# Optimization experiments

Measured on AMD Instinct MI355X. Metric: run time of the kernel, lower is better.

Reference implementation:

```python
import jax, jax.numpy as jnp
import numpy as np

B, T, IN_DIM, EMB = 8, 2048, 1024, 1024
NEG_INF = -1e30  # stand-in for float('-inf'); exp() underflows to 0 identically


def setup_inputs() -> dict:
    key = jax.random.key(0)
    ks = jax.random.split(key, 7)
    s = 1.0 / np.sqrt(IN_DIM)
    return {
        "x": jax.random.normal(ks[0], (B, T, IN_DIM), dtype=jnp.float32),
        "Wq": jax.random.normal(ks[1], (IN_DIM, EMB), dtype=jnp.float32) * s,
        "bq": jax.random.normal(ks[2], (EMB,), dtype=jnp.float32) * 0.01,
        "Wk": jax.random.normal(ks[3], (IN_DIM, EMB), dtype=jnp.float32) * s,
        "bk": jax.random.normal(ks[4], (EMB,), dtype=jnp.float32) * 0.01,
        "Wv": jax.random.normal(ks[5], (IN_DIM, EMB), dtype=jnp.float32) * s,
        "bv": jax.random.normal(ks[6], (EMB,), dtype=jnp.float32) * 0.01,
    }


def reference(x, Wq, bq, Wk, bk, Wv, bv):
    # projections: [B, T, EMB]
    q = x @ Wq + bq
    k = x @ Wk + bk
    v = x @ Wv + bv
    scale = jnp.asarray(EMB, x.dtype) ** 0.5
    # scores: [B, T, T]
    scores = jnp.einsum("btd,bsd->bts", q, k) / scale
    Tq = scores.shape[-2]
    causal = jnp.tril(jnp.ones((Tq, Tq), dtype=bool))  # [T, T]
    scores = jnp.where(causal, scores, jnp.asarray(NEG_INF, scores.dtype))
    # Faithful to torch.vmap(softmax): per-batch GLOBAL-matrix softmax
    # (max and sum taken over the whole [T, T] matrix, not per row).
    m = jnp.max(scores, axis=(-2, -1), keepdims=True)
    e = jnp.exp(scores - m)
    w = e / jnp.sum(e, axis=(-2, -1), keepdims=True)
    # output: [B, T, EMB]
    return jnp.einsum("bts,bsd->btd", w, v)
```

## Files before the change

### kernel.cpp

```cpp
#include <hip/hip_runtime.h>
#include <stdint.h>


#define B_   8
#define T_   2048
#define DIM  1024

typedef _Float16 f16;
typedef f16   f16x8 __attribute__((ext_vector_type(8)));
typedef f16   f16x4 __attribute__((ext_vector_type(4)));
typedef float f32x4 __attribute__((ext_vector_type(4)));

typedef const __attribute__((address_space(1))) void gvoid_t;
typedef __attribute__((address_space(3))) void lvoid_t;

__device__ __forceinline__ void stage128x32(const uint16_t* __restrict__ g, int ld,
                                            uint16_t* s, int tid) {
#pragma unroll
  for (int c = 0; c < 2; ++c) {
    int r    = (tid >> 2) + 64 * c;
    int gseg = (tid & 3) ^ ((r >> 1) & 3);
    const uint16_t* gp = g + (size_t)r * ld + gseg * 8;
    uint16_t* sp = s + c * 2048 + (tid >> 6) * 512;
    __builtin_amdgcn_global_load_lds((gvoid_t*)gp, (lvoid_t*)sp, 16, 0, 0);
  }
}

__device__ __forceinline__ f16x8 fragld(const uint16_t* s, int row, int quad) {
  int seg = quad ^ ((row >> 1) & 3);
  return *(const f16x8*)(s + row * 32 + seg * 8);
}

__device__ __forceinline__ void gemm_f16(const uint16_t* gA, const uint16_t* gB,
                                         int lda, int ldb, int ksteps,
                                         uint16_t* smem, f32x4 acc[4][4]) {
  const int tid = threadIdx.x, lane = tid & 63, wv = tid >> 6;
  const int quad = lane >> 4, l15 = lane & 15;
  const int moff = (wv >> 1) * 64, noff = (wv & 1) * 64;
  uint16_t* sA = smem;
  uint16_t* sB = smem + 4096;
#pragma unroll 1
  for (int ks = 0; ks < ksteps; ++ks) {
    if (ks) __syncthreads();
    stage128x32(gA + ks * 32, lda, sA, tid);
    stage128x32(gB + ks * 32, ldb, sB, tid);
    __syncthreads();
    f16x8 a[4], b[4];
#pragma unroll
    for (int i = 0; i < 4; ++i) {
      a[i] = fragld(sA, moff + i * 16 + l15, quad);
      b[i] = fragld(sB, noff + i * 16 + l15, quad);
    }
#pragma unroll
    for (int mi = 0; mi < 4; ++mi)
#pragma unroll
      for (int ni = 0; ni < 4; ++ni)
        acc[mi][ni] = __builtin_amdgcn_mfma_f32_16x16x32_f16(a[mi], b[ni], acc[mi][ni], 0, 0, 0);
  }
}

__device__ __forceinline__ void zero_acc(f32x4 acc[4][4]) {
  f32x4 z = {0.f, 0.f, 0.f, 0.f};
#pragma unroll
  for (int i = 0; i < 4; ++i)
#pragma unroll
    for (int j = 0; j < 4; ++j) acc[i][j] = z;
}


__device__ __forceinline__ void stage_half256(const uint16_t* __restrict__ g, int ld,
                                              uint16_t* s, int tid) {
#pragma unroll
  for (int j = 0; j < 2; ++j) {
    int r   = j * 64 + (tid >> 3);
    int seg = (tid & 7) ^ (r & 7);
    const uint16_t* gp = g + (size_t)r * ld + seg * 8;
    uint16_t* sp = s + j * 4096 + (tid >> 6) * 512;
    __builtin_amdgcn_global_load_lds((gvoid_t*)gp, (lvoid_t*)sp, 16, 0, 0);
  }
}

__device__ __forceinline__ f16x8 frag64(const uint16_t* s, int r, int gseg) {
  return *(const f16x8*)(s + r * 64 + ((gseg ^ (r & 7)) * 8));
}

__device__ __forceinline__ void lda4(const uint16_t* s, int rbase, int quad, int l15,
                                     f16x8 o[4][2]) {
#pragma unroll
  for (int mf = 0; mf < 4; ++mf) {
    int r = rbase + mf * 16 + l15;
#pragma unroll
    for (int kk = 0; kk < 2; ++kk) o[mf][kk] = frag64(s, r, kk * 4 + quad);
  }
}

__device__ __forceinline__ void ldb2(const uint16_t* s, int rbase, int quad, int l15,
                                     f16x8 o[2][2]) {
#pragma unroll
  for (int nf = 0; nf < 2; ++nf) {
    int r = rbase + nf * 16 + l15;
#pragma unroll
    for (int kk = 0; kk < 2; ++kk) o[nf][kk] = frag64(s, r, kk * 4 + quad);
  }
}

template <int M0, int N0>
__device__ __forceinline__ void mm16(f16x8 a[4][2], f16x8 b[2][2], f32x4 (&acc)[8][4]) {
#pragma unroll
  for (int kk = 0; kk < 2; ++kk)
#pragma unroll
    for (int mf = 0; mf < 4; ++mf)
#pragma unroll
      for (int nf = 0; nf < 2; ++nf)
        acc[M0 + mf][N0 + nf] = __builtin_amdgcn_mfma_f32_16x16x32_f16(
            a[mf][kk], b[nf][kk], acc[M0 + mf][N0 + nf], 0, 0, 0);
}

#define SYNC_MFMA(AA, BB, M0, N0)                      \
  __builtin_amdgcn_s_barrier();                        \
  asm volatile("s_waitcnt lgkmcnt(0)" ::: "memory");   \
  __builtin_amdgcn_s_setprio(1);                       \
  mm16<M0, N0>(AA, BB, acc);                           \
  __builtin_amdgcn_s_setprio(0);                       \
  __builtin_amdgcn_s_barrier();


__global__ void zero_lrow_kernel(float* __restrict__ lrow) {
  lrow[blockIdx.x * 256 + threadIdx.x] = 0.f;
}

__global__ void conv_x_kernel(const float* __restrict__ x, f16* __restrict__ xf) {
  size_t i = (size_t)blockIdx.x * 256 + threadIdx.x;
  float4 v = ((const float4*)x)[i];
  f16x4 o = {(f16)v.x, (f16)v.y, (f16)v.z, (f16)v.w};
  ((f16x4*)xf)[i] = o;
}

__global__ void convT_w_kernel(const float* __restrict__ Wq, const float* __restrict__ Wk,
                               const float* __restrict__ Wv, f16* __restrict__ WT) {
  __shared__ float tile[64][65];
  const int z = blockIdx.z;
  const float* W = (z == 0) ? Wq : (z == 1) ? Wk : Wv;
  const int r0 = blockIdx.x * 64, c0 = blockIdx.y * 64, tid = threadIdx.x;
#pragma unroll
  for (int i = 0; i < 16; ++i) {
    int rr = (tid >> 6) + 4 * i, cc = tid & 63;
    tile[rr][cc] = W[(size_t)(r0 + rr) * DIM + c0 + cc];
  }
  __syncthreads();
#pragma unroll
  for (int i = 0; i < 16; ++i) {
    int nn = (tid >> 6) + 4 * i, kk = tid & 63;
    WT[(size_t)z * DIM * DIM + (size_t)(c0 + nn) * DIM + r0 + kk] = (f16)tile[kk][nn];
  }
}

__global__ void reduce_z_kernel(const float* __restrict__ lrow, float* __restrict__ invZ) {
  const int b = blockIdx.x, tid = threadIdx.x;
  float s = 0.f;
  for (int i = tid; i < T_; i += 256) s += lrow[(size_t)b * T_ + i];
#pragma unroll
  for (int off = 1; off < 64; off <<= 1) s += __shfl_xor(s, off, 64);
  __shared__ float red[4];
  if ((tid & 63) == 0) red[tid >> 6] = s;
  __syncthreads();
  if (tid == 0) invZ[b] = 1.0f / (red[0] + red[1] + red[2] + red[3]);
}


__global__ __launch_bounds__(512, 2) void proj_kernel(
    const f16* __restrict__ xf, const f16* __restrict__ WT,
    const float* __restrict__ bq, const float* __restrict__ bk, const float* __restrict__ bv,
    f16* __restrict__ q, f16* __restrict__ k, f16* __restrict__ vT) {
  __shared__ uint16_t smem[65536];

  const int bid = blockIdx.x;
  const int sw  = (bid & 7) * 96 + (bid >> 3);
  const int z = sw >> 8, by = (sw >> 6) & 3, bx = sw & 63;
  const size_t arow = (size_t)bx * 256;
  const int    bcol = by * 256;
  const uint16_t* gA = (const uint16_t*)xf + arow * DIM;
  const uint16_t* gB = (const uint16_t*)WT + (size_t)z * DIM * DIM + (size_t)bcol * DIM;

  const int tid = threadIdx.x, lane = tid & 63, wv = tid >> 6;
  const int quad = lane >> 4, l15 = lane & 15;
  const int wr = wv >> 2, wc = wv & 3;

  uint16_t* sA0 = smem;
  uint16_t* sA1 = smem + 16384;
  uint16_t* sB0 = smem + 32768;
  uint16_t* sB1 = smem + 49152;

  f32x4 acc[8][4];
  {
    f32x4 zz = {0.f, 0.f, 0.f, 0.f};
#pragma unroll
    for (int i = 0; i < 8; ++i)
#pragma unroll
      for (int j = 0; j < 4; ++j) acc[i][j] = zz;
  }

  stage_half256(gA,                 DIM, sA0,        tid);
  stage_half256(gA + 128 * DIM,     DIM, sA0 + 8192, tid);
  stage_half256(gB,                 DIM, sB0,        tid);
  stage_half256(gB + 128 * DIM,     DIM, sB0 + 8192, tid);
  stage_half256(gB + 64,            DIM, sB1,        tid);
  stage_half256(gB + 64 + 128 * DIM, DIM, sB1 + 8192, tid);
  asm volatile("s_waitcnt vmcnt(4)" ::: "memory");
  __builtin_amdgcn_s_barrier();

  f16x8 alo[4][2], ahi[4][2], blo[2][2], bhi[2][2];
#pragma unroll 1
  for (int it = 0; it < 8; ++it) {
    const int t1 = 2 * it + 1;
    int t2 = 2 * it + 2; if (t2 > 15) t2 = 15;
    int t3 = 2 * it + 3; if (t3 > 15) t3 = 15;
    const uint16_t* gA1 = gA + t1 * 64;
    const uint16_t* gA2 = gA + t2 * 64;
    const uint16_t* gB2 = gB + t2 * 64;
    const uint16_t* gB3 = gB + t3 * 64;

    lda4(sA0, wr * 128,      quad, l15, alo);
    ldb2(sB0, wc * 64,       quad, l15, blo);
    stage_half256(gA1, DIM, sA1, tid);
    SYNC_MFMA(alo, blo, 0, 0)
    ldb2(sB0, wc * 64 + 32,  quad, l15, bhi);
    stage_half256(gA1 + 128 * DIM, DIM, sA1 + 8192, tid);
    SYNC_MFMA(alo, bhi, 0, 2)
    lda4(sA0, wr * 128 + 64, quad, l15, ahi);
    stage_half256(gB2, DIM, sB0, tid);
    SYNC_MFMA(ahi, bhi, 4, 2)
    stage_half256(gB2 + 128 * DIM, DIM, sB0 + 8192, tid);
    asm volatile("s_waitcnt vmcnt(4)" ::: "memory");
    SYNC_MFMA(ahi, blo, 4, 0)
    lda4(sA1, wr * 128,      quad, l15, alo);
    ldb2(sB1, wc * 64,       quad, l15, blo);
    stage_half256(gA2, DIM, sA0, tid);
    SYNC_MFMA(alo, blo, 0, 0)
    ldb2(sB1, wc * 64 + 32,  quad, l15, bhi);
    stage_half256(gA2 + 128 * DIM, DIM, sA0 + 8192, tid);
    SYNC_MFMA(alo, bhi, 0, 2)
    lda4(sA1, wr * 128 + 64, quad, l15, ahi);
    stage_half256(gB3, DIM, sB1, tid);
    SYNC_MFMA(ahi, bhi, 4, 2)
    stage_half256(gB3 + 128 * DIM, DIM, sB1 + 8192, tid);
    asm volatile("s_waitcnt vmcnt(4)" ::: "memory");
    SYNC_MFMA(ahi, blo, 4, 0)
  }

  const float* bias = (z == 0) ? bq : (z == 1) ? bk : bv;
  if (z < 2) {
    f16* O = z ? k : q;
#pragma unroll
    for (int mf = 0; mf < 8; ++mf)
#pragma unroll
      for (int nf = 0; nf < 4; ++nf) {
        int n = bcol + wc * 64 + nf * 16 + l15;
        float bb = bias[n];
        size_t row0 = arow + wr * 128 + mf * 16 + quad * 4;
#pragma unroll
        for (int r = 0; r < 4; ++r)
          O[(row0 + r) * DIM + n] = (f16)(acc[mf][nf][r] + bb);
      }
  } else {
#pragma unroll
    for (int mf = 0; mf < 8; ++mf)
#pragma unroll
      for (int nf = 0; nf < 4; ++nf) {
        int n = bcol + wc * 64 + nf * 16 + l15;
        float bb = bias[n];
        int row0 = (int)arow + wr * 128 + mf * 16 + quad * 4;
        int bb_i = row0 >> 11, t0 = row0 & 2047;
        f16x4 pk;
#pragma unroll
        for (int r = 0; r < 4; ++r) pk[r] = (f16)(acc[mf][nf][r] + bb);
        *(f16x4*)(vT + ((size_t)bb_i * DIM + n) * T_ + t0) = pk;
      }
  }
}

__global__ __launch_bounds__(256, 2) void scores_kernel(
    const f16* __restrict__ q, const f16* __restrict__ k,
    f16* __restrict__ E, float* __restrict__ lrow) {
  const int qi = blockIdx.x, ki = blockIdx.y, b = blockIdx.z;
  if (ki > qi) return;
  __shared__ uint16_t smem[8192];
  f32x4 acc[4][4];
  zero_acc(acc);
  const size_t aoff = ((size_t)b * T_ + qi * 128) * DIM;
  const size_t boff = ((size_t)b * T_ + ki * 128) * DIM;
  gemm_f16((const uint16_t*)(q + aoff), (const uint16_t*)(k + boff), DIM, DIM, DIM / 32, smem, acc);

  const int tid = threadIdx.x, lane = tid & 63, wv = tid >> 6;
  const int quad = lane >> 4, l15 = lane & 15;
  const int moff = (wv >> 1) * 64, noff = (wv & 1) * 64;
  f16*   Eb = E + (size_t)b * T_ * T_;
  float* lb = lrow + (size_t)b * T_;
  const bool diag = (ki == qi);
#pragma unroll
  for (int mi = 0; mi < 4; ++mi) {
    float rs[4] = {0.f, 0.f, 0.f, 0.f};
#pragma unroll
    for (int ni = 0; ni < 4; ++ni)
#pragma unroll
      for (int r = 0; r < 4; ++r) {
        int t = qi * 128 + moff + mi * 16 + quad * 4 + r;
        int s = ki * 128 + noff + ni * 16 + l15;
        float e = 0.f;
        if (!diag || s <= t) e = __expf(fminf(acc[mi][ni][r] * 0.03125f, 11.f));
        Eb[(size_t)t * T_ + s] = (f16)e;
        rs[r] += e;
      }
#pragma unroll
    for (int off = 1; off < 16; off <<= 1)
#pragma unroll
      for (int r = 0; r < 4; ++r) rs[r] += __shfl_xor(rs[r], off, 64);
    if (l15 == 0)
#pragma unroll
      for (int r = 0; r < 4; ++r)
        atomicAdd(&lb[qi * 128 + moff + mi * 16 + quad * 4 + r], rs[r]);
  }
}

__global__ __launch_bounds__(256, 2) void pv_kernel(
    const f16* __restrict__ E, const f16* __restrict__ vT,
    const float* __restrict__ invZ, float* __restrict__ out) {
  const int qi = blockIdx.x, nt = blockIdx.y, b = blockIdx.z;
  __shared__ uint16_t smem[8192];
  f32x4 acc[4][4];
  zero_acc(acc);
  gemm_f16((const uint16_t*)(E + ((size_t)b * T_ + qi * 128) * (size_t)T_),
           (const uint16_t*)(vT + ((size_t)b * DIM + nt * 128) * (size_t)T_),
           T_, T_, (qi + 1) * 4, smem, acc);
  const float iz = invZ[b];
  const int tid = threadIdx.x, lane = tid & 63, wv = tid >> 6;
  const int quad = lane >> 4, l15 = lane & 15;
  const int moff = (wv >> 1) * 64, noff = (wv & 1) * 64;
  float* ob = out + (size_t)b * T_ * DIM;
#pragma unroll
  for (int mi = 0; mi < 4; ++mi)
#pragma unroll
    for (int ni = 0; ni < 4; ++ni)
#pragma unroll
      for (int r = 0; r < 4; ++r) {
        int t = qi * 128 + moff + mi * 16 + quad * 4 + r;
        int n = nt * 128 + noff + ni * 16 + l15;
        ob[(size_t)t * DIM + n] = acc[mi][ni][r] * iz;
      }
}


extern "C" void kernel_launch(void* const* d_in, const int* in_sizes, int n_in,
                              void* d_out, int out_size, void* d_ws, size_t ws_size,
                              hipStream_t stream) {
  const float* x  = (const float*)d_in[0];
  const float* Wq = (const float*)d_in[1];
  const float* bq = (const float*)d_in[2];
  const float* Wk = (const float*)d_in[3];
  const float* bk = (const float*)d_in[4];
  const float* Wv = (const float*)d_in[5];
  const float* bv = (const float*)d_in[6];
  float* out = (float*)d_out;

  const size_t SZ = (size_t)B_ * T_ * DIM;
  char* ws = (char*)d_ws;
  f16*   E    = (f16*)ws;
  f16*   xf   = (f16*)ws;
  f16*   q    = (f16*)(ws + 67108864);
  f16*   k    = (f16*)(ws + 100663296);
  f16*   vT   = (f16*)(ws + 134217728);
  f16*   WT   = (f16*)(ws + 167772160);
  float* lrow = (float*)(ws + 174063616);
  float* invZ = (float*)(ws + 174129152);
  if (ws_size < (size_t)174129184) return;

  zero_lrow_kernel<<<64, 256, 0, stream>>>(lrow);
  conv_x_kernel<<<16384, 256, 0, stream>>>(x, xf);
  convT_w_kernel<<<dim3(16, 16, 3), 256, 0, stream>>>(Wq, Wk, Wv, WT);
  proj_kernel<<<dim3(768), 512, 0, stream>>>(xf, WT, bq, bk, bv, q, k, vT);
  scores_kernel<<<dim3(16, 16, 8), 256, 0, stream>>>(q, k, E, lrow);
  reduce_z_kernel<<<B_, 256, 0, stream>>>(lrow, invZ);
  pv_kernel<<<dim3(16, 8, 8), 256, 0, stream>>>(E, vT, invZ, out);
}
```

Before: 417.2 us.

## Reuse pipelined 256x256 GEMM core for scores and PV kernels

Pulls the double-buffered 8-phase 256x256 GEMM loop out of the projection kernel into a shared helper. The scores and PV kernels now use it in place of the simple 128x128 single-buffered GEMM. Scores launches only the lower-triangle tiles through a linear index with XCD-aware batch mapping, and the projection block mapping is reordered. Larger tiles and prefetching raise data reuse and MFMA utilisation, but give fewer blocks (288 and 256) and coarser causal load imbalance in PV.

```diff
diff --git a/kernel.cpp b/kernel.cpp
--- a/kernel.cpp
+++ b/kernel.cpp
@@ -13,59 +13,6 @@
 
 typedef const __attribute__((address_space(1))) void gvoid_t;
 typedef __attribute__((address_space(3))) void lvoid_t;
-
-__device__ __forceinline__ void stage128x32(const uint16_t* __restrict__ g, int ld,
-                                            uint16_t* s, int tid) {
-#pragma unroll
-  for (int c = 0; c < 2; ++c) {
-    int r    = (tid >> 2) + 64 * c;
-    int gseg = (tid & 3) ^ ((r >> 1) & 3);
-    const uint16_t* gp = g + (size_t)r * ld + gseg * 8;
-    uint16_t* sp = s + c * 2048 + (tid >> 6) * 512;
-    __builtin_amdgcn_global_load_lds((gvoid_t*)gp, (lvoid_t*)sp, 16, 0, 0);
-  }
-}
-
-__device__ __forceinline__ f16x8 fragld(const uint16_t* s, int row, int quad) {
-  int seg = quad ^ ((row >> 1) & 3);
-  return *(const f16x8*)(s + row * 32 + seg * 8);
-}
-
-__device__ __forceinline__ void gemm_f16(const uint16_t* gA, const uint16_t* gB,
-                                         int lda, int ldb, int ksteps,
-                                         uint16_t* smem, f32x4 acc[4][4]) {
-  const int tid = threadIdx.x, lane = tid & 63, wv = tid >> 6;
-  const int quad = lane >> 4, l15 = lane & 15;
-  const int moff = (wv >> 1) * 64, noff = (wv & 1) * 64;
-  uint16_t* sA = smem;
-  uint16_t* sB = smem + 4096;
-#pragma unroll 1
-  for (int ks = 0; ks < ksteps; ++ks) {
-    if (ks) __syncthreads();
-    stage128x32(gA + ks * 32, lda, sA, tid);
-    stage128x32(gB + ks * 32, ldb, sB, tid);
-    __syncthreads();
-    f16x8 a[4], b[4];
-#pragma unroll
-    for (int i = 0; i < 4; ++i) {
-      a[i] = fragld(sA, moff + i * 16 + l15, quad);
-      b[i] = fragld(sB, noff + i * 16 + l15, quad);
-    }
-#pragma unroll
-    for (int mi = 0; mi < 4; ++mi)
-#pragma unroll
-      for (int ni = 0; ni < 4; ++ni)
-        acc[mi][ni] = __builtin_amdgcn_mfma_f32_16x16x32_f16(a[mi], b[ni], acc[mi][ni], 0, 0, 0);
-  }
-}
-
-__device__ __forceinline__ void zero_acc(f32x4 acc[4][4]) {
-  f32x4 z = {0.f, 0.f, 0.f, 0.f};
-#pragma unroll
-  for (int i = 0; i < 4; ++i)
-#pragma unroll
-    for (int j = 0; j < 4; ++j) acc[i][j] = z;
-}
 
 
 __device__ __forceinline__ void stage_half256(const uint16_t* __restrict__ g, int ld,
@@ -124,6 +71,77 @@
   __builtin_amdgcn_s_setprio(0);                       \
   __builtin_amdgcn_s_barrier();
 
+__device__ __forceinline__ void gemm256_8ph(const uint16_t* __restrict__ gA,
+                                            const uint16_t* __restrict__ gB,
+                                            int lda, int ldb, int nIter,
+                                            uint16_t* smem, f32x4 (&acc)[8][4]) {
+  const int tid = threadIdx.x, lane = tid & 63, wv = tid >> 6;
+  const int quad = lane >> 4, l15 = lane & 15;
+  const int wr = wv >> 2, wc = wv & 3;
+
+  uint16_t* sA0 = smem;
+  uint16_t* sA1 = smem + 16384;
+  uint16_t* sB0 = smem + 32768;
+  uint16_t* sB1 = smem + 49152;
+
+  stage_half256(gA,                        lda, sA0,        tid);
+  stage_half256(gA + 128 * (size_t)lda,    lda, sA0 + 8192, tid);
+  stage_half256(gB,                        ldb, sB0,        tid);
+  stage_half256(gB + 128 * (size_t)ldb,    ldb, sB0 + 8192, tid);
+  stage_half256(gB + 64,                   ldb, sB1,        tid);
+  stage_half256(gB + 64 + 128 * (size_t)ldb, ldb, sB1 + 8192, tid);
+  asm volatile("s_waitcnt vmcnt(4)" ::: "memory");
+  __builtin_amdgcn_s_barrier();
+
+  f16x8 alo[4][2], ahi[4][2], blo[2][2], bhi[2][2];
+  const int tmax = 2 * nIter - 1;
+#pragma unroll 1
+  for (int it = 0; it < nIter; ++it) {
+    const int t1 = 2 * it + 1;
+    int t2 = 2 * it + 2; if (t2 > tmax) t2 = tmax;
+    int t3 = 2 * it + 3; if (t3 > tmax) t3 = tmax;
+    const uint16_t* gA1 = gA + t1 * 64;
+    const uint16_t* gA2 = gA + t2 * 64;
+    const uint16_t* gB2 = gB + t2 * 64;
+    const uint16_t* gB3 = gB + t3 * 64;
+
+    lda4(sA0, wr * 128,      quad, l15, alo);
+    ldb2(sB0, wc * 64,       quad, l15, blo);
+    stage_half256(gA1, lda, sA1, tid);
+    SYNC_MFMA(alo, blo, 0, 0)
+    ldb2(sB0, wc * 64 + 32,  quad, l15, bhi);
+    stage_half256(gA1 + 128 * (size_t)lda, lda, sA1 + 8192, tid);
+    SYNC_MFMA(alo, bhi, 0, 2)
+    lda4(sA0, wr * 128 + 64, quad, l15, ahi);
+    stage_half256(gB2, ldb, sB0, tid);
+    SYNC_MFMA(ahi, bhi, 4, 2)
+    stage_half256(gB2 + 128 * (size_t)ldb, ldb, sB0 + 8192, tid);
+    asm volatile("s_waitcnt vmcnt(4)" ::: "memory");
+    SYNC_MFMA(ahi, blo, 4, 0)
+    lda4(sA1, wr * 128,      quad, l15, alo);
+    ldb2(sB1, wc * 64,       quad, l15, blo);
+    stage_half256(gA2, lda, sA0, tid);
+    SYNC_MFMA(alo, blo, 0, 0)
+    ldb2(sB1, wc * 64 + 32,  quad, l15, bhi);
+    stage_half256(gA2 + 128 * (size_t)lda, lda, sA0 + 8192, tid);
+    SYNC_MFMA(alo, bhi, 0, 2)
+    lda4(sA1, wr * 128 + 64, quad, l15, ahi);
+    stage_half256(gB3, ldb, sB1, tid);
+    SYNC_MFMA(ahi, bhi, 4, 2)
+    stage_half256(gB3 + 128 * (size_t)ldb, ldb, sB1 + 8192, tid);
+    asm volatile("s_waitcnt vmcnt(4)" ::: "memory");
+    SYNC_MFMA(ahi, blo, 4, 0)
+  }
+}
+
+__device__ __forceinline__ void zero_acc8(f32x4 (&acc)[8][4]) {
+  f32x4 z = {0.f, 0.f, 0.f, 0.f};
+#pragma unroll
+  for (int i = 0; i < 8; ++i)
+#pragma unroll
+    for (int j = 0; j < 4; ++j) acc[i][j] = z;
+}
+
 
 __global__ void zero_lrow_kernel(float* __restrict__ lrow) {
   lrow[blockIdx.x * 256 + threadIdx.x] = 0.f;
@@ -175,80 +193,23 @@
   __shared__ uint16_t smem[65536];
 
   const int bid = blockIdx.x;
-  const int sw  = (bid & 7) * 96 + (bid >> 3);
-  const int z = sw >> 8, by = (sw >> 6) & 3, bx = sw & 63;
+  const int xcd = bid & 7, local = bid >> 3;
+  const int bx = xcd * 8 + (local & 7);
+  const int zy = local >> 3;
+  const int z = zy >> 2, by = zy & 3;
   const size_t arow = (size_t)bx * 256;
   const int    bcol = by * 256;
-  const uint16_t* gA = (const uint16_t*)xf + arow * DIM;
-  const uint16_t* gB = (const uint16_t*)WT + (size_t)z * DIM * DIM + (size_t)bcol * DIM;
-
+
+  f32x4 acc[8][4];
+  zero_acc8(acc);
+  gemm256_8ph((const uint16_t*)xf + arow * DIM,
+              (const uint16_t*)WT + (size_t)z * DIM * DIM + (size_t)bcol * DIM,
+              DIM, DIM, 8, smem, acc);
+
+  const float* bias = (z == 0) ? bq : (z == 1) ? bk : bv;
   const int tid = threadIdx.x, lane = tid & 63, wv = tid >> 6;
   const int quad = lane >> 4, l15 = lane & 15;
   const int wr = wv >> 2, wc = wv & 3;
-
-  uint16_t* sA0 = smem;
-  uint16_t* sA1 = smem + 16384;
-  uint16_t* sB0 = smem + 32768;
-  uint16_t* sB1 = smem + 49152;
-
-  f32x4 acc[8][4];
-  {
-    f32x4 zz = {0.f, 0.f, 0.f, 0.f};
-#pragma unroll
-    for (int i = 0; i < 8; ++i)
-#pragma unroll
-      for (int j = 0; j < 4; ++j) acc[i][j] = zz;
-  }
-
-  stage_half256(gA,                 DIM, sA0,        tid);
-  stage_half256(gA + 128 * DIM,     DIM, sA0 + 8192, tid);
-  stage_half256(gB,                 DIM, sB0,        tid);
-  stage_half256(gB + 128 * DIM,     DIM, sB0 + 8192, tid);
-  stage_half256(gB + 64,            DIM, sB1,        tid);
-  stage_half256(gB + 64 + 128 * DIM, DIM, sB1 + 8192, tid);
-  asm volatile("s_waitcnt vmcnt(4)" ::: "memory");
-  __builtin_amdgcn_s_barrier();
-
-  f16x8 alo[4][2], ahi[4][2], blo[2][2], bhi[2][2];
-#pragma unroll 1
-  for (int it = 0; it < 8; ++it) {
-    const int t1 = 2 * it + 1;
-    int t2 = 2 * it + 2; if (t2 > 15) t2 = 15;
-    int t3 = 2 * it + 3; if (t3 > 15) t3 = 15;
-    const uint16_t* gA1 = gA + t1 * 64;
-    const uint16_t* gA2 = gA + t2 * 64;
-    const uint16_t* gB2 = gB + t2 * 64;
-    const uint16_t* gB3 = gB + t3 * 64;
-
-    lda4(sA0, wr * 128,      quad, l15, alo);
-    ldb2(sB0, wc * 64,       quad, l15, blo);
-    stage_half256(gA1, DIM, sA1, tid);
-    SYNC_MFMA(alo, blo, 0, 0)
-    ldb2(sB0, wc * 64 + 32,  quad, l15, bhi);
-    stage_half256(gA1 + 128 * DIM, DIM, sA1 + 8192, tid);
-    SYNC_MFMA(alo, bhi, 0, 2)
-    lda4(sA0, wr * 128 + 64, quad, l15, ahi);
-    stage_half256(gB2, DIM, sB0, tid);
-    SYNC_MFMA(ahi, bhi, 4, 2)
-    stage_half256(gB2 + 128 * DIM, DIM, sB0 + 8192, tid);
-    asm volatile("s_waitcnt vmcnt(4)" ::: "memory");
-    SYNC_MFMA(ahi, blo, 4, 0)
-    lda4(sA1, wr * 128,      quad, l15, alo);
-    ldb2(sB1, wc * 64,       quad, l15, blo);
-    stage_half256(gA2, DIM, sA0, tid);
-    SYNC_MFMA(alo, blo, 0, 0)
-    ldb2(sB1, wc * 64 + 32,  quad, l15, bhi);
-    stage_half256(gA2 + 128 * DIM, DIM, sA0 + 8192, tid);
-    SYNC_MFMA(alo, bhi, 0, 2)
-    lda4(sA1, wr * 128 + 64, quad, l15, ahi);
-    stage_half256(gB3, DIM, sB1, tid);
-    SYNC_MFMA(ahi, bhi, 4, 2)
-    stage_half256(gB3 + 128 * DIM, DIM, sB1 + 8192, tid);
-    asm volatile("s_waitcnt vmcnt(4)" ::: "memory");
-    SYNC_MFMA(ahi, blo, 4, 0)
-  }
-
-  const float* bias = (z == 0) ? bq : (z == 1) ? bk : bv;
   if (z < 2) {
     f16* O = z ? k : q;
 #pragma unroll
@@ -279,35 +240,39 @@
   }
 }
 
-__global__ __launch_bounds__(256, 2) void scores_kernel(
+__global__ __launch_bounds__(512, 2) void scores_kernel(
     const f16* __restrict__ q, const f16* __restrict__ k,
     f16* __restrict__ E, float* __restrict__ lrow) {
-  const int qi = blockIdx.x, ki = blockIdx.y, b = blockIdx.z;
-  if (ki > qi) return;
-  __shared__ uint16_t smem[8192];
-  f32x4 acc[4][4];
-  zero_acc(acc);
-  const size_t aoff = ((size_t)b * T_ + qi * 128) * DIM;
-  const size_t boff = ((size_t)b * T_ + ki * 128) * DIM;
-  gemm_f16((const uint16_t*)(q + aoff), (const uint16_t*)(k + boff), DIM, DIM, DIM / 32, smem, acc);
+  __shared__ uint16_t smem[65536];
+  const int bid = blockIdx.x;
+  const int b = bid & 7, tri = bid >> 3;
+  int qi = 0;
+  while ((qi + 1) * (qi + 2) / 2 <= tri) ++qi;
+  const int ki = tri - qi * (qi + 1) / 2;
+
+  f32x4 acc[8][4];
+  zero_acc8(acc);
+  gemm256_8ph((const uint16_t*)(q + ((size_t)b * T_ + qi * 256) * DIM),
+              (const uint16_t*)(k + ((size_t)b * T_ + ki * 256) * DIM),
+              DIM, DIM, 8, smem, acc);
 
   const int tid = threadIdx.x, lane = tid & 63, wv = tid >> 6;
   const int quad = lane >> 4, l15 = lane & 15;
-  const int moff = (wv >> 1) * 64, noff = (wv & 1) * 64;
+  const int wr = wv >> 2, wc = wv & 3;
   f16*   Eb = E + (size_t)b * T_ * T_;
   float* lb = lrow + (size_t)b * T_;
   const bool diag = (ki == qi);
 #pragma unroll
-  for (int mi = 0; mi < 4; ++mi) {
+  for (int mf = 0; mf < 8; ++mf) {
     float rs[4] = {0.f, 0.f, 0.f, 0.f};
 #pragma unroll
-    for (int ni = 0; ni < 4; ++ni)
+    for (int nf = 0; nf < 4; ++nf)
 #pragma unroll
       for (int r = 0; r < 4; ++r) {
-        int t = qi * 128 + moff + mi * 16 + quad * 4 + r;
-        int s = ki * 128 + noff + ni * 16 + l15;
+        int t = qi * 256 + wr * 128 + mf * 16 + quad * 4 + r;
+        int s = ki * 256 + wc * 64 + nf * 16 + l15;
         float e = 0.f;
-        if (!diag || s <= t) e = __expf(fminf(acc[mi][ni][r] * 0.03125f, 11.f));
+        if (!diag || s <= t) e = __expf(fminf(acc[mf][nf][r] * 0.03125f, 11.f));
         Eb[(size_t)t * T_ + s] = (f16)e;
         rs[r] += e;
       }
@@ -318,34 +283,38 @@
     if (l15 == 0)
 #pragma unroll
       for (int r = 0; r < 4; ++r)
-        atomicAdd(&lb[qi * 128 + moff + mi * 16 + quad * 4 + r], rs[r]);
-  }
-}
-
-__global__ __launch_bounds__(256, 2) void pv_kernel(
+        atomicAdd(&lb[qi * 256 + wr * 128 + mf * 16 + quad * 4 + r], rs[r]);
+  }
+}
+
+__global__ __launch_bounds__(512, 2) void pv_kernel(
     const f16* __restrict__ E, const f16* __restrict__ vT,
     const float* __restrict__ invZ, float* __restrict__ out) {
-  const int qi = blockIdx.x, nt = blockIdx.y, b = blockIdx.z;
-  __shared__ uint16_t smem[8192];
-  f32x4 acc[4][4];
-  zero_acc(acc);
-  gemm_f16((const uint16_t*)(E + ((size_t)b * T_ + qi * 128) * (size_t)T_),
-           (const uint16_t*)(vT + ((size_t)b * DIM + nt * 128) * (size_t)T_),
-           T_, T_, (qi + 1) * 4, smem, acc);
+  __shared__ uint16_t smem[65536];
+  const int bid = blockIdx.x;
+  const int b = bid & 7, local = bid >> 3;
+  const int qi = local & 7, nt = local >> 3;
+
+  f32x4 acc[8][4];
+  zero_acc8(acc);
+  gemm256_8ph((const uint16_t*)(E + ((size_t)b * T_ + qi * 256) * (size_t)T_),
+              (const uint16_t*)(vT + ((size_t)b * DIM + nt * 256) * (size_t)T_),
+              T_, T_, (qi + 1) * 2, smem, acc);
+
   const float iz = invZ[b];
   const int tid = threadIdx.x, lane = tid & 63, wv = tid >> 6;
   const int quad = lane >> 4, l15 = lane & 15;
-  const int moff = (wv >> 1) * 64, noff = (wv & 1) * 64;
+  const int wr = wv >> 2, wc = wv & 3;
   float* ob = out + (size_t)b * T_ * DIM;
 #pragma unroll
-  for (int mi = 0; mi < 4; ++mi)
-#pragma unroll
-    for (int ni = 0; ni < 4; ++ni)
+  for (int mf = 0; mf < 8; ++mf)
+#pragma unroll
+    for (int nf = 0; nf < 4; ++nf)
 #pragma unroll
       for (int r = 0; r < 4; ++r) {
-        int t = qi * 128 + moff + mi * 16 + quad * 4 + r;
-        int n = nt * 128 + noff + ni * 16 + l15;
-        ob[(size_t)t * DIM + n] = acc[mi][ni][r] * iz;
+        int t = qi * 256 + wr * 128 + mf * 16 + quad * 4 + r;
+        int n = nt * 256 + wc * 64 + nf * 16 + l15;
+        ob[(size_t)t * DIM + n] = acc[mf][nf][r] * iz;
       }
 }
 
@@ -362,7 +331,6 @@
   const float* bv = (const float*)d_in[6];
   float* out = (float*)d_out;
 
-  const size_t SZ = (size_t)B_ * T_ * DIM;
   char* ws = (char*)d_ws;
   f16*   E    = (f16*)ws;
   f16*   xf   = (f16*)ws;
@@ -378,7 +346,7 @@
   conv_x_kernel<<<16384, 256, 0, stream>>>(x, xf);
   convT_w_kernel<<<dim3(16, 16, 3), 256, 0, stream>>>(Wq, Wk, Wv, WT);
   proj_kernel<<<dim3(768), 512, 0, stream>>>(xf, WT, bq, bk, bv, q, k, vT);
-  scores_kernel<<<dim3(16, 16, 8), 256, 0, stream>>>(q, k, E, lrow);
+  scores_kernel<<<dim3(288), 512, 0, stream>>>(q, k, E, lrow);
   reduce_z_kernel<<<B_, 256, 0, stream>>>(lrow, invZ);
-  pv_kernel<<<dim3(16, 8, 8), 256, 0, stream>>>(E, vT, invZ, out);
-}
+  pv_kernel<<<dim3(256), 512, 0, stream>>>(E, vT, invZ, out);
+}
```

Measured after the change: 353.5 us. -15.3%, faster.
